# Optimization experiments

Hardware: AMD Instinct MI355X
Metric: run time of the kernel (lower is better)

## Reference

```python
import jax, jax.numpy as jnp
import numpy as np

EPS = 1e-5


def sage_conv(x, src, dst, Wl, Wr, b, n):
    # PyG SAGEConv: out_i = W_l * mean_{j in N(i)} x_j + W_r * x_i + b
    agg = jax.ops.segment_sum(x[src], dst, num_segments=n)  # [N, d]
    deg = jax.ops.segment_sum(jnp.ones_like(src, dtype=x.dtype), dst, num_segments=n)
    agg = agg / jnp.maximum(deg, 1.0)[:, None]
    return agg @ Wl + x @ Wr + b


def setup_inputs() -> dict:
    key = jax.random.key(0)
    ks = jax.random.split(key, 12)
    N, E, D_IN, D_H, D_OUT = 50000, 600000, 128, 128, 64
    x = jax.random.normal(ks[0], (N, D_IN), dtype=jnp.float32)
    edge_index = jax.random.randint(ks[1], (2, E), 0, N, dtype=jnp.int64)
    s_in = 1.0 / np.sqrt(D_IN)
    s_h = 1.0 / np.sqrt(D_H)
    return {
        "x": x,
        "edge_index": edge_index,
        "Wl0": jax.random.normal(ks[2], (D_IN, D_H), jnp.float32) * s_in,
        "Wr0": jax.random.normal(ks[3], (D_IN, D_H), jnp.float32) * s_in,
        "b0": jnp.zeros((D_H,), jnp.float32),
        "Wl1": jax.random.normal(ks[4], (D_H, D_H), jnp.float32) * s_h,
        "Wr1": jax.random.normal(ks[5], (D_H, D_H), jnp.float32) * s_h,
        "b1": jnp.zeros((D_H,), jnp.float32),
        "Wl2": jax.random.normal(ks[6], (D_H, D_OUT), jnp.float32) * s_h,
        "Wr2": jax.random.normal(ks[7], (D_H, D_OUT), jnp.float32) * s_h,
        "b2": jnp.zeros((D_OUT,), jnp.float32),
        "gamma": jnp.ones((D_H,), jnp.float32),
        "beta": jnp.zeros((D_H,), jnp.float32),
    }


def reference(x, edge_index, Wl0, Wr0, b0, Wl1, Wr1, b1, Wl2, Wr2, b2, gamma, beta):
    n = x.shape[0]
    src, dst = edge_index[0], edge_index[1]
    residual = x  # in_channels == hidden_channels -> no residual_transform
    # layer 0: conv + relu (+ dropout as identity in eval)
    h = jax.nn.relu(sage_conv(x, src, dst, Wl0, Wr0, b0, n))
    # middle layer: conv + BN(batch stats) + relu + residual
    h = sage_conv(h, src, dst, Wl1, Wr1, b1, n)
    mu = jnp.mean(h, axis=0)
    var = jnp.var(h, axis=0)  # biased, as in torch BN normalization
    h = (h - mu) * jax.lax.rsqrt(var + EPS) * gamma + beta
    h = jax.nn.relu(h) + residual
    # output layer
    h = sage_conv(h, src, dst, Wl2, Wr2, b2, n)
    return jax.nn.log_softmax(h, axis=-1)
```

## Files before the change

kernel.cpp:

```cpp
#include <hip/hip_runtime.h>
#include <hip/hip_bf16.h>


#define WS_EPS 1e-5f

typedef unsigned short ushort_t;
typedef unsigned int uint_t;
typedef unsigned char uchar_t;
typedef ushort_t ushort8 __attribute__((ext_vector_type(8)));
typedef short short8 __attribute__((ext_vector_type(8)));
typedef float f32x4 __attribute__((ext_vector_type(4)));
typedef _Float16 half2v __attribute__((ext_vector_type(2)));

__device__ __forceinline__ float bf2f(ushort_t u) {
    return __uint_as_float(((uint_t)u) << 16);
}
__device__ __forceinline__ ushort_t f2bf(float f) {
    uint_t u = __float_as_uint(f);
    u = (u + 0x7fffu + ((u >> 16) & 1u)) >> 16;
    return (ushort_t)u;
}
__device__ __forceinline__ uchar_t f2e4m3(float f) {
    _Float16 hf = (_Float16)f;
    uint_t h = (uint_t)__builtin_bit_cast(unsigned short, hf);
    uint_t s = (h >> 8) & 0x80u;
    uint_t r = h & 0x7fffu;
    if (r < 0x2400u) return (uchar_t)0;
    if (r > 0x5F40u) r = 0x5F00u;
    uint_t u = r - 0x2000u;
    uint_t m = (u + 0x3fu + ((u >> 7) & 1u)) >> 7;
    return (uchar_t)(s | m);
}

constexpr int SCHUNK = 4096;

__global__ __launch_bounds__(256) void k_scan_part(const int* __restrict__ deg,
                                                   int* __restrict__ bsum, int n) {
    int t = threadIdx.x;
    int base = blockIdx.x * SCHUNK + t * 16;
    int s = 0;
#pragma unroll
    for (int j = 0; j < 16; ++j) {
        int i = base + j;
        if (i < n) s += deg[i];
    }
#pragma unroll
    for (int d = 1; d < 64; d <<= 1) s += __shfl_xor(s, d);
    __shared__ int wt[4];
    if ((t & 63) == 0) wt[t >> 6] = s;
    __syncthreads();
    if (t == 0) bsum[blockIdx.x] = wt[0] + wt[1] + wt[2] + wt[3];
}

__global__ __launch_bounds__(64) void k_scan_bsum(const int* __restrict__ bsum,
                                                  int* __restrict__ boff,
                                                  int* __restrict__ off_n, int nb) {
    int lane = threadIdx.x;
    int carry = 0;
    for (int base = 0; base < nb; base += 64) {
        int t = base + lane;
        int v = (t < nb) ? bsum[t] : 0;
        int x = v;
#pragma unroll
        for (int d = 1; d < 64; d <<= 1) {
            int y = __shfl_up(x, d);
            if (lane >= d) x += y;
        }
        if (t < nb) boff[t] = carry + x - v;
        carry += __shfl(x, 63);
    }
    if (lane == 0) *off_n = carry;
}

__global__ __launch_bounds__(256) void k_scan_apply(const int* __restrict__ deg,
                                                    const int* __restrict__ boff,
                                                    int* __restrict__ off, int n) {
    int t = threadIdx.x;
    int lane = t & 63, wid = t >> 6;
    int base = blockIdx.x * SCHUNK + t * 16;
    int v[16];
    int s = 0;
#pragma unroll
    for (int j = 0; j < 16; ++j) {
        int i = base + j;
        v[j] = (i < n) ? deg[i] : 0;
        s += v[j];
    }
    int x = s;
#pragma unroll
    for (int d = 1; d < 64; d <<= 1) {
        int y = __shfl_up(x, d);
        if (lane >= d) x += y;
    }
    __shared__ int wtot[4];
    if (lane == 63) wtot[wid] = x;
    __syncthreads();
    int woff = 0;
    for (int wj = 0; wj < wid; ++wj) woff += wtot[wj];
    int run = boff[blockIdx.x] + woff + x - s;
#pragma unroll
    for (int j = 0; j < 16; ++j) {
        int i = base + j;
        if (i < n) off[i] = run;
        run += v[j];
    }
}

__global__ __launch_bounds__(256) void k_scatter(const int* __restrict__ ei,
                                                 const int* __restrict__ off,
                                                 int* __restrict__ cur,
                                                 int* __restrict__ csr, int E) {
    int e = blockIdx.x * 256 + threadIdx.x;
    if (e < E) {
        int d = ei[E + e];
        int s = ei[e];
        int p = atomicAdd(&cur[d], 1);
        csr[off[d] + p] = s;
    }
}

__global__ __launch_bounds__(256) void k_deg_prep(const int* __restrict__ ei,
                                                  int* __restrict__ deg, int E, int eb,
                                                  const float* __restrict__ x,
                                                  ushort_t* __restrict__ xb,
                                                  uchar_t* __restrict__ x8,
                                                  int total2, int nb_cvt,
                                                  const float* __restrict__ Wl0,
                                                  const float* __restrict__ Wr0,
                                                  const float* __restrict__ Wl1,
                                                  const float* __restrict__ Wr1,
                                                  const float* __restrict__ Wl2,
                                                  const float* __restrict__ Wr2,
                                                  ushort_t* __restrict__ wts) {
    int b = blockIdx.x;
    if (b < eb) {
        int e = b * 256 + threadIdx.x;
        if (e < E) atomicAdd(&deg[ei[E + e]], 1);
        return;
    }
    b -= eb;
    if (b < nb_cvt) {
        int i = b * 256 + threadIdx.x;
        if (i >= total2) return;
        float2 v = *(const float2*)&x[(size_t)i * 2];
        uint_t p = (uint_t)f2bf(v.x) | ((uint_t)f2bf(v.y) << 16);
        *(uint_t*)&xb[(size_t)i * 2] = p;
        ushort_t q = (ushort_t)((uint_t)f2e4m3(v.x) | ((uint_t)f2e4m3(v.y) << 8));
        *(ushort_t*)&x8[(size_t)i * 2] = q;
        return;
    }
    int id = (b - nb_cvt) * 256 + threadIdx.x;
    if (id >= 81920) return;
    const float* W;
    int rel, nout, base;
    if (id < 65536) {
        int m = id >> 14;
        rel = id & 16383;
        nout = 128;
        base = m << 14;
        W = (m == 0) ? Wl0 : (m == 1) ? Wr0 : (m == 2) ? Wl1 : Wr1;
    } else {
        int m = (id - 65536) >> 13;
        rel = (id - 65536) & 8191;
        nout = 64;
        base = 65536 + (m << 13);
        W = (m == 0) ? Wl2 : Wr2;
    }
    int c = rel >> 7;
    int k = rel & 127;
    wts[base + rel] = f2bf(W[(size_t)k * nout + c]);
}

template <int EPI>
__global__ __launch_bounds__(256, 3) void k_dgemm(const ushort_t* __restrict__ X1,
                                                  const ushort_t* __restrict__ W1,
                                                  const ushort_t* __restrict__ X2,
                                                  const ushort_t* __restrict__ W2,
                                                  const float* __restrict__ bias,
                                                  ushort_t* __restrict__ outp,
                                                  uchar_t* __restrict__ out8,
                                                  float* __restrict__ stats, int n) {
    constexpr int K = 128, NOUT = 128;
    __shared__ ushort_t Bs[2048 * 8];
    __shared__ float sred[256];

    const int t = threadIdx.x;
    const int lane = t & 63;
    const int r16 = lane & 15, kb = lane >> 4;
    const int half = blockIdx.x & 1;
    const int colbase = half * 64;
    const int w = t >> 6;
    const int sA = (blockIdx.x >> 1) * 8 + w * 2;
    const int sB = sA + 1;

    if (EPI == 1) sred[t] = 0.f;

    ushort8 wreg[8];
#pragma unroll
    for (int u = 0; u < 8; ++u) {
        int slot = u * 256 + t;
        int mat = slot >> 10;
        int rem = slot & 1023;
        int fnks = rem >> 6;
        int l = rem & 63;
        int fn = fnks >> 2, ks = fnks & 3;
        const ushort_t* Wm = mat ? W2 : W1;
        wreg[u] = *(const ushort8*)&Wm[(size_t)(colbase + fn * 16 + (l & 15)) * K +
                                       ks * 32 + (l >> 4) * 8];
    }
    const int rowA = sA * 16 + r16, rowB = sB * 16 + r16;
    const bool okA = rowA < n, okB = rowB < n;
    const size_t xoA = (size_t)rowA * K + kb * 8;
    const size_t xoB = (size_t)rowB * K + kb * 8;
    short8 a1A[4], a2A[4], a1B[4], a2B[4];
#pragma unroll
    for (int ks = 0; ks < 4; ++ks)
        a1A[ks] = okA ? *(const short8*)&X1[xoA + ks * 32] : (short8)0;
#pragma unroll
    for (int ks = 0; ks < 4; ++ks)
        a2A[ks] = okA ? *(const short8*)&X2[xoA + ks * 32] : (short8)0;
#pragma unroll
    for (int ks = 0; ks < 4; ++ks)
        a1B[ks] = okB ? *(const short8*)&X1[xoB + ks * 32] : (short8)0;
#pragma unroll
    for (int ks = 0; ks < 4; ++ks)
        a2B[ks] = okB ? *(const short8*)&X2[xoB + ks * 32] : (short8)0;
#pragma unroll
    for (int u = 0; u < 8; ++u) {
        int slot = u * 256 + t;
        *(ushort8*)&Bs[(size_t)slot * 8] = wreg[u];
    }
    __syncthreads();

    f32x4 accA[4] = {(f32x4)0.f, (f32x4)0.f, (f32x4)0.f, (f32x4)0.f};
    f32x4 accB[4] = {(f32x4)0.f, (f32x4)0.f, (f32x4)0.f, (f32x4)0.f};
#pragma unroll
    for (int ks = 0; ks < 4; ++ks)
#pragma unroll
        for (int fn = 0; fn < 4; ++fn) {
            short8 b = *(const short8*)&Bs[((fn * 4 + ks) * 64 + lane) * 8];
            accA[fn] = __builtin_amdgcn_mfma_f32_16x16x32_bf16(a1A[ks], b, accA[fn], 0, 0, 0);
            accB[fn] = __builtin_amdgcn_mfma_f32_16x16x32_bf16(a1B[ks], b, accB[fn], 0, 0, 0);
        }
#pragma unroll
    for (int ks = 0; ks < 4; ++ks)
#pragma unroll
        for (int fn = 0; fn < 4; ++fn) {
            short8 b = *(const short8*)&Bs[((16 + fn * 4 + ks) * 64 + lane) * 8];
            accA[fn] = __builtin_amdgcn_mfma_f32_16x16x32_bf16(a2A[ks], b, accA[fn], 0, 0, 0);
            accB[fn] = __builtin_amdgcn_mfma_f32_16x16x32_bf16(a2B[ks], b, accB[fn], 0, 0, 0);
        }

    float bcol[4];
#pragma unroll
    for (int fn = 0; fn < 4; ++fn) bcol[fn] = bias[colbase + fn * 16 + r16];

    float ssum[4] = {0.f, 0.f, 0.f, 0.f}, qsum[4] = {0.f, 0.f, 0.f, 0.f};

    {
        const int rb = sA * 16 + kb * 4;
#pragma unroll
        for (int r = 0; r < 4; ++r) {
            int row = rb + r;
            if (row >= n) continue;
#pragma unroll
            for (int fn = 0; fn < 4; ++fn) {
                int col = colbase + fn * 16 + r16;
                float v = accA[fn][r] + bcol[fn];
                if constexpr (EPI == 2) {
                    v = fmaxf(v, 0.f);
                    outp[(size_t)row * NOUT + col] = f2bf(v);
                    out8[(size_t)row * NOUT + col] = f2e4m3(v);
                } else {
                    outp[(size_t)row * NOUT + col] = f2bf(v);
                    ssum[fn] += v;
                    qsum[fn] += v * v;
                }
            }
        }
    }
    {
        const int rb = sB * 16 + kb * 4;
#pragma unroll
        for (int r = 0; r < 4; ++r) {
            int row = rb + r;
            if (row >= n) continue;
#pragma unroll
            for (int fn = 0; fn < 4; ++fn) {
                int col = colbase + fn * 16 + r16;
                float v = accB[fn][r] + bcol[fn];
                if constexpr (EPI == 2) {
                    v = fmaxf(v, 0.f);
                    outp[(size_t)row * NOUT + col] = f2bf(v);
                    out8[(size_t)row * NOUT + col] = f2e4m3(v);
                } else {
                    outp[(size_t)row * NOUT + col] = f2bf(v);
                    ssum[fn] += v;
                    qsum[fn] += v * v;
                }
            }
        }
    }

    if constexpr (EPI == 1) {
#pragma unroll
        for (int fn = 0; fn < 4; ++fn) {
            ssum[fn] += __shfl_xor(ssum[fn], 16);
            ssum[fn] += __shfl_xor(ssum[fn], 32);
            qsum[fn] += __shfl_xor(qsum[fn], 16);
            qsum[fn] += __shfl_xor(qsum[fn], 32);
        }
        if (kb == 0) {
#pragma unroll
            for (int fn = 0; fn < 4; ++fn) {
                int col = colbase + fn * 16 + r16;
                atomicAdd(&sred[col], ssum[fn]);
                atomicAdd(&sred[128 + col], qsum[fn]);
            }
        }
        __syncthreads();
        atomicAdd(&stats[t], sred[t]);
    }
}

__global__ __launch_bounds__(256, 4) void k_cgemm(const ushort_t* __restrict__ H,
                                                  const ushort_t* __restrict__ WL,
                                                  const ushort_t* __restrict__ WR,
                                                  const float* __restrict__ b2,
                                                  ushort_t* __restrict__ A64,
                                                  ushort_t* __restrict__ Tb, int n) {
    constexpr int K = 128;
    __shared__ ushort_t Bs[2048 * 8];

    const int t = threadIdx.x;
    const int lane = t & 63;
    const int r16 = lane & 15, kb = lane >> 4;
    const int strip = blockIdx.x * 4 + (t >> 6);

    ushort8 wreg[8];
#pragma unroll
    for (int u = 0; u < 8; ++u) {
        int slot = u * 256 + t;
        int mat = slot >> 10;
        int rem = slot & 1023;
        int fnks = rem >> 6;
        int l = rem & 63;
        int fn = fnks >> 2, ks = fnks & 3;
        const ushort_t* Wm = mat ? WR : WL;
        wreg[u] = *(const ushort8*)&Wm[(size_t)(fn * 16 + (l & 15)) * K +
                                       ks * 32 + (l >> 4) * 8];
    }
    const int arow = strip * 16 + r16;
    const bool rok = (arow < n);
    const size_t xo = (size_t)arow * K + kb * 8;
    short8 a[4];
#pragma unroll
    for (int ks = 0; ks < 4; ++ks)
        a[ks] = rok ? *(const short8*)&H[xo + ks * 32] : (short8)0;
#pragma unroll
    for (int u = 0; u < 8; ++u) {
        int slot = u * 256 + t;
        *(ushort8*)&Bs[(size_t)slot * 8] = wreg[u];
    }
    __syncthreads();

    f32x4 aL[4] = {(f32x4)0.f, (f32x4)0.f, (f32x4)0.f, (f32x4)0.f};
    f32x4 aR[4] = {(f32x4)0.f, (f32x4)0.f, (f32x4)0.f, (f32x4)0.f};
#pragma unroll
    for (int ks = 0; ks < 4; ++ks)
#pragma unroll
        for (int fn = 0; fn < 4; ++fn) {
            short8 bl = *(const short8*)&Bs[((fn * 4 + ks) * 64 + lane) * 8];
            short8 br = *(const short8*)&Bs[((16 + fn * 4 + ks) * 64 + lane) * 8];
            aL[fn] = __builtin_amdgcn_mfma_f32_16x16x32_bf16(a[ks], bl, aL[fn], 0, 0, 0);
            aR[fn] = __builtin_amdgcn_mfma_f32_16x16x32_bf16(a[ks], br, aR[fn], 0, 0, 0);
        }

    float bcol[4];
#pragma unroll
    for (int fn = 0; fn < 4; ++fn) bcol[fn] = b2[fn * 16 + r16];

    const int rb = strip * 16 + kb * 4;
#pragma unroll
    for (int r = 0; r < 4; ++r) {
        int row = rb + r;
        if (row >= n) continue;
#pragma unroll
        for (int fn = 0; fn < 4; ++fn) {
            int col = fn * 16 + r16;
            A64[(size_t)row * 64 + col] = f2bf(aL[fn][r]);
            Tb[(size_t)row * 64 + col] = f2bf(aR[fn][r] + bcol[fn]);
        }
    }
}

__global__ __launch_bounds__(256) void k_segmean8(const uchar_t* __restrict__ U8,
                                                  const int* __restrict__ off,
                                                  const int* __restrict__ srcs,
                                                  ushort_t* __restrict__ out, int n) {
    int node = blockIdx.x * 32 + (threadIdx.x >> 3);
    int sub = threadIdx.x & 7;
    if (node >= n) return;
    int beg = off[node], end = off[node + 1];
    half2v aE0 = (half2v)0, aE1 = (half2v)0, aE2 = (half2v)0, aE3 = (half2v)0;
    half2v aO0 = (half2v)0, aO1 = (half2v)0, aO2 = (half2v)0, aO3 = (half2v)0;

#define DEC(dw, AE, AO)                                                           \
    {                                                                             \
        uint_t xe = (dw)&0x00ff00ffu;                                             \
        uint_t xo = ((dw) >> 8) & 0x00ff00ffu;                                    \
        uint_t he = ((xe & 0x00800080u) << 8) |                                   \
                    (((xe & 0x007f007fu) << 7) + 0x20002000u);                    \
        uint_t ho = ((xo & 0x00800080u) << 8) |                                   \
                    (((xo & 0x007f007fu) << 7) + 0x20002000u);                    \
        AE += __builtin_bit_cast(half2v, he);                                     \
        AO += __builtin_bit_cast(half2v, ho);                                     \
    }

    auto addrow = [&](int sidx) {
        uint4 v = *(const uint4*)&U8[(size_t)sidx * 128 + sub * 16];
        DEC(v.x, aE0, aO0)
        DEC(v.y, aE1, aO1)
        DEC(v.z, aE2, aO2)
        DEC(v.w, aE3, aO3)
    };
#undef DEC

    int i = beg;
    for (; i + 8 <= end; i += 8) {
        int sv[8];
#pragma unroll
        for (int u = 0; u < 8; ++u) sv[u] = srcs[i + u];
#pragma unroll
        for (int u = 0; u < 8; ++u) addrow(sv[u]);
    }
    for (; i < end; ++i) addrow(srcs[i]);

    int d = end - beg;
    float inv = 1.f / (float)(d > 1 ? d : 1);
    ushort8 o0, o1;
#define PACK(AE, AO, O, IDX)                     \
    O[IDX] = f2bf((float)AE[0] * inv);           \
    O[IDX + 1] = f2bf((float)AO[0] * inv);       \
    O[IDX + 2] = f2bf((float)AE[1] * inv);       \
    O[IDX + 3] = f2bf((float)AO[1] * inv);
    PACK(aE0, aO0, o0, 0)
    PACK(aE1, aO1, o0, 4)
    PACK(aE2, aO2, o1, 0)
    PACK(aE3, aO3, o1, 4)
#undef PACK
    *(ushort8*)&out[(size_t)node * 128 + sub * 16] = o0;
    *(ushort8*)&out[(size_t)node * 128 + sub * 16 + 8] = o1;
}

__global__ __launch_bounds__(256) void k_segmean_lsm(const ushort_t* __restrict__ A64,
                                                     const int* __restrict__ off,
                                                     const int* __restrict__ srcs,
                                                     const ushort_t* __restrict__ Tb,
                                                     float* __restrict__ out, int n) {
    int node = blockIdx.x * 32 + (threadIdx.x >> 3);
    int sub = threadIdx.x & 7;
    if (node >= n) return;
    int beg = off[node], end = off[node + 1];
    float a[8];
#pragma unroll
    for (int j = 0; j < 8; ++j) a[j] = 0.f;
    int i = beg;
    for (; i + 8 <= end; i += 8) {
        int sv[8];
#pragma unroll
        for (int u = 0; u < 8; ++u) sv[u] = srcs[i + u];
#pragma unroll
        for (int u = 0; u < 8; ++u) {
            ushort8 v = *(const ushort8*)&A64[(size_t)sv[u] * 64 + sub * 8];
#pragma unroll
            for (int j = 0; j < 8; ++j) a[j] += bf2f((ushort_t)v[j]);
        }
    }
    for (; i < end; ++i) {
        ushort8 v = *(const ushort8*)&A64[(size_t)srcs[i] * 64 + sub * 8];
#pragma unroll
        for (int j = 0; j < 8; ++j) a[j] += bf2f((ushort_t)v[j]);
    }
    int d = end - beg;
    float inv = 1.f / (float)(d > 1 ? d : 1);
    ushort8 tv = *(const ushort8*)&Tb[(size_t)node * 64 + sub * 8];
    float vv[8];
#pragma unroll
    for (int j = 0; j < 8; ++j) vv[j] = a[j] * inv + bf2f((ushort_t)tv[j]);
    float m = vv[0];
#pragma unroll
    for (int j = 1; j < 8; ++j) m = fmaxf(m, vv[j]);
#pragma unroll
    for (int dd = 1; dd < 8; dd <<= 1) m = fmaxf(m, __shfl_xor(m, dd));
    float e = 0.f;
#pragma unroll
    for (int j = 0; j < 8; ++j) e += expf(vv[j] - m);
#pragma unroll
    for (int dd = 1; dd < 8; dd <<= 1) e += __shfl_xor(e, dd);
    float lg = m + logf(e);
    f32x4 o0, o1;
#pragma unroll
    for (int j = 0; j < 4; ++j) {
        o0[j] = vv[j] - lg;
        o1[j] = vv[4 + j] - lg;
    }
    *(f32x4*)&out[(size_t)node * 64 + sub * 8] = o0;
    *(f32x4*)&out[(size_t)node * 64 + sub * 8 + 4] = o1;
}

__global__ __launch_bounds__(256) void k_bnapply(const ushort_t* __restrict__ P,
                                                 const ushort_t* __restrict__ Xb,
                                                 const float* __restrict__ stats,
                                                 const float* __restrict__ gamma,
                                                 const float* __restrict__ beta,
                                                 ushort_t* __restrict__ H, int n) {
    int i = blockIdx.x * 256 + threadIdx.x;
    if (i >= n * 64) return;
    int nd = i >> 6;
    int c = (i & 63) << 1;
    float inv_n = 1.f / (float)n;
    float mu0 = stats[c] * inv_n, mu1 = stats[c + 1] * inv_n;
    float v0 = stats[128 + c] * inv_n - mu0 * mu0;
    float v1 = stats[128 + c + 1] * inv_n - mu1 * mu1;
    float s0 = rsqrtf(v0 + WS_EPS) * gamma[c];
    float s1 = rsqrtf(v1 + WS_EPS) * gamma[c + 1];
    uint_t pv = *(const uint_t*)&P[(size_t)nd * 128 + c];
    uint_t xv = *(const uint_t*)&Xb[(size_t)nd * 128 + c];
    float p0 = __uint_as_float(pv << 16);
    float p1 = __uint_as_float(pv & 0xffff0000u);
    float x0 = __uint_as_float(xv << 16);
    float x1 = __uint_as_float(xv & 0xffff0000u);
    float h0 = fmaxf((p0 - mu0) * s0 + beta[c], 0.f) + x0;
    float h1 = fmaxf((p1 - mu1) * s1 + beta[c + 1], 0.f) + x1;
    uint_t pk = (uint_t)f2bf(h0) | ((uint_t)f2bf(h1) << 16);
    *(uint_t*)&H[(size_t)nd * 128 + c] = pk;
}

extern "C" void kernel_launch(void* const* d_in, const int* in_sizes, int n_in,
                              void* d_out, int out_size, void* d_ws, size_t ws_size,
                              hipStream_t stream) {
    const float* x     = (const float*)d_in[0];
    const int*   ei    = (const int*)d_in[1];
    const float* Wl0   = (const float*)d_in[2];
    const float* Wr0   = (const float*)d_in[3];
    const float* b0    = (const float*)d_in[4];
    const float* Wl1   = (const float*)d_in[5];
    const float* Wr1   = (const float*)d_in[6];
    const float* b1    = (const float*)d_in[7];
    const float* Wl2   = (const float*)d_in[8];
    const float* Wr2   = (const float*)d_in[9];
    const float* b2    = (const float*)d_in[10];
    const float* gamma = (const float*)d_in[11];
    const float* beta  = (const float*)d_in[12];

    const int n = in_sizes[0] / 128;
    const int E = in_sizes[1] / 2;
    const int nb_scan = (n + SCHUNK - 1) / SCHUNK;

    char* w = (char*)d_ws;
    auto alloc = [&](size_t bytes) -> void* {
        void* p = (void*)w;
        w += (bytes + 255) & ~(size_t)255;
        return p;
    };
    int*      deg   = (int*)alloc((size_t)n * 4);
    int*      cur   = (int*)alloc((size_t)n * 4);
    float*    stats = (float*)alloc(256 * 4);
    size_t    zbytes = (size_t)((char*)w - (char*)deg);
    int*      off   = (int*)alloc(((size_t)n + 1) * 4);
    int*      csr   = (int*)alloc((size_t)E * 4);
    int*      bsum  = (int*)alloc(256 * 4);
    int*      boff  = (int*)alloc(256 * 4);
    ushort_t* wts   = (ushort_t*)alloc((size_t)81920 * 2);
    ushort_t* xb    = (ushort_t*)alloc((size_t)n * 128 * 2);
    uchar_t*  x8    = (uchar_t*)alloc((size_t)n * 128);
    ushort_t* H     = (ushort_t*)alloc((size_t)n * 128 * 2);
    uchar_t*  H8    = (uchar_t*)alloc((size_t)n * 128);
    ushort_t* Pb    = (ushort_t*)alloc((size_t)n * 128 * 2);
    ushort_t* M     = (ushort_t*)alloc((size_t)n * 128 * 2);
    ushort_t* A64   = (ushort_t*)alloc((size_t)n * 64 * 2);
    ushort_t* Tb    = (ushort_t*)alloc((size_t)n * 64 * 2);

    ushort_t* WtL0 = wts;
    ushort_t* WtR0 = wts + 16384;
    ushort_t* WtL1 = wts + 32768;
    ushort_t* WtR1 = wts + 49152;
    ushort_t* WtL2 = wts + 65536;
    ushort_t* WtR2 = wts + 73728;

    hipMemsetAsync(deg, 0, zbytes, stream);

    const int eb = (E + 255) / 256;
    const int nb_cvt = (n * 64 + 255) / 256;
    k_deg_prep<<<eb + nb_cvt + 320, 256, 0, stream>>>(ei, deg, E, eb, x, xb, x8,
                                                      n * 64, nb_cvt,
                                                      Wl0, Wr0, Wl1, Wr1, Wl2, Wr2, wts);
    k_scan_part<<<nb_scan, 256, 0, stream>>>(deg, bsum, n);
    k_scan_bsum<<<1, 64, 0, stream>>>(bsum, boff, off + n, nb_scan);
    k_scan_apply<<<nb_scan, 256, 0, stream>>>(deg, boff, off, n);
    k_scatter<<<(E + 255) / 256, 256, 0, stream>>>(ei, off, cur, csr, E);

    const int strips = (n + 15) / 16;
    const int gb_d = 2 * ((strips + 7) / 8);
    const int gb_c = (strips + 3) / 4;
    const int smb = (n + 31) / 32;

    k_segmean8<<<smb, 256, 0, stream>>>(x8, off, csr, M, n);
    k_dgemm<2><<<gb_d, 256, 0, stream>>>(xb, WtR0, M, WtL0, b0, H, H8, nullptr, n);

    k_segmean8<<<smb, 256, 0, stream>>>(H8, off, csr, M, n);
    k_dgemm<1><<<gb_d, 256, 0, stream>>>(H, WtR1, M, WtL1, b1, Pb, nullptr, stats, n);
    k_bnapply<<<(n * 64 + 255) / 256, 256, 0, stream>>>(Pb, xb, stats, gamma, beta, H, n);

    k_cgemm<<<gb_c, 256, 0, stream>>>(H, WtL2, WtR2, b2, A64, Tb, n);
    k_segmean_lsm<<<smb, 256, 0, stream>>>(A64, off, csr, Tb, (float*)d_out, n);
}
```

Before: 224.9 us.

## Fuse BN-apply into output GEMM and double rows per dgemm wave

```diff
diff --git a/kernel.cpp b/kernel.cpp
--- a/kernel.cpp
+++ b/kernel.cpp
@@ -171,8 +171,42 @@
     wts[base + rel] = f2bf(W[(size_t)k * nout + c]);
 }
 
+#define DG_LOADA(A1, A2, SS)                                                   \
+    {                                                                          \
+        int row_ = (SS)*16 + r16;                                              \
+        bool ok_ = row_ < n;                                                   \
+        size_t xo_ = (size_t)row_ * K + kb * 8;                                \
+        _Pragma("unroll") for (int ks = 0; ks < 4; ++ks)                       \
+            A1[ks] = ok_ ? *(const short8*)&X1[xo_ + ks * 32] : (short8)0;     \
+        _Pragma("unroll") for (int ks = 0; ks < 4; ++ks)                       \
+            A2[ks] = ok_ ? *(const short8*)&X2[xo_ + ks * 32] : (short8)0;     \
+    }
+
+#define DG_EPI(ACC, SS)                                                        \
+    {                                                                          \
+        const int rb_ = (SS)*16 + kb * 4;                                      \
+        _Pragma("unroll") for (int r = 0; r < 4; ++r) {                        \
+            int row_ = rb_ + r;                                                \
+            if (row_ < n) {                                                    \
+                _Pragma("unroll") for (int fn = 0; fn < 4; ++fn) {             \
+                    int col_ = colbase + fn * 16 + r16;                        \
+                    float v_ = ACC[fn][r] + bcol[fn];                          \
+                    if (EPI == 2) {                                            \
+                        v_ = fmaxf(v_, 0.f);                                   \
+                        outp[(size_t)row_ * NOUT + col_] = f2bf(v_);           \
+                        out8[(size_t)row_ * NOUT + col_] = f2e4m3(v_);         \
+                    } else {                                                   \
+                        outp[(size_t)row_ * NOUT + col_] = f2bf(v_);           \
+                        ssum[fn] += v_;                                        \
+                        qsum[fn] += v_ * v_;                                   \
+                    }                                                          \
+                }                                                              \
+            }                                                                  \
+        }                                                                      \
+    }
+
 template <int EPI>
-__global__ __launch_bounds__(256, 3) void k_dgemm(const ushort_t* __restrict__ X1,
+__global__ __launch_bounds__(256, 2) void k_dgemm(const ushort_t* __restrict__ X1,
                                                   const ushort_t* __restrict__ W1,
                                                   const ushort_t* __restrict__ X2,
                                                   const ushort_t* __restrict__ W2,
@@ -190,8 +224,8 @@
     const int half = blockIdx.x & 1;
     const int colbase = half * 64;
     const int w = t >> 6;
-    const int sA = (blockIdx.x >> 1) * 8 + w * 2;
-    const int sB = sA + 1;
+    const int sA = (blockIdx.x >> 1) * 16 + w * 4;
+    const int sB = sA + 1, sC = sA + 2, sD = sA + 3;
 
     if (EPI == 1) sred[t] = 0.f;
 
@@ -208,23 +242,11 @@
         wreg[u] = *(const ushort8*)&Wm[(size_t)(colbase + fn * 16 + (l & 15)) * K +
                                        ks * 32 + (l >> 4) * 8];
     }
-    const int rowA = sA * 16 + r16, rowB = sB * 16 + r16;
-    const bool okA = rowA < n, okB = rowB < n;
-    const size_t xoA = (size_t)rowA * K + kb * 8;
-    const size_t xoB = (size_t)rowB * K + kb * 8;
-    short8 a1A[4], a2A[4], a1B[4], a2B[4];
-#pragma unroll
-    for (int ks = 0; ks < 4; ++ks)
-        a1A[ks] = okA ? *(const short8*)&X1[xoA + ks * 32] : (short8)0;
-#pragma unroll
-    for (int ks = 0; ks < 4; ++ks)
-        a2A[ks] = okA ? *(const short8*)&X2[xoA + ks * 32] : (short8)0;
-#pragma unroll
-    for (int ks = 0; ks < 4; ++ks)
-        a1B[ks] = okB ? *(const short8*)&X1[xoB + ks * 32] : (short8)0;
-#pragma unroll
-    for (int ks = 0; ks < 4; ++ks)
-        a2B[ks] = okB ? *(const short8*)&X2[xoB + ks * 32] : (short8)0;
+    short8 a1A[4], a2A[4], a1B[4], a2B[4], a1C[4], a2C[4], a1D[4], a2D[4];
+    DG_LOADA(a1A, a2A, sA)
+    DG_LOADA(a1B, a2B, sB)
+    DG_LOADA(a1C, a2C, sC)
+    DG_LOADA(a1D, a2D, sD)
 #pragma unroll
     for (int u = 0; u < 8; ++u) {
         int slot = u * 256 + t;
@@ -234,6 +256,8 @@
 
     f32x4 accA[4] = {(f32x4)0.f, (f32x4)0.f, (f32x4)0.f, (f32x4)0.f};
     f32x4 accB[4] = {(f32x4)0.f, (f32x4)0.f, (f32x4)0.f, (f32x4)0.f};
+    f32x4 accC[4] = {(f32x4)0.f, (f32x4)0.f, (f32x4)0.f, (f32x4)0.f};
+    f32x4 accD[4] = {(f32x4)0.f, (f32x4)0.f, (f32x4)0.f, (f32x4)0.f};
 #pragma unroll
     for (int ks = 0; ks < 4; ++ks)
 #pragma unroll
@@ -241,6 +265,8 @@
             short8 b = *(const short8*)&Bs[((fn * 4 + ks) * 64 + lane) * 8];
             accA[fn] = __builtin_amdgcn_mfma_f32_16x16x32_bf16(a1A[ks], b, accA[fn], 0, 0, 0);
             accB[fn] = __builtin_amdgcn_mfma_f32_16x16x32_bf16(a1B[ks], b, accB[fn], 0, 0, 0);
+            accC[fn] = __builtin_amdgcn_mfma_f32_16x16x32_bf16(a1C[ks], b, accC[fn], 0, 0, 0);
+            accD[fn] = __builtin_amdgcn_mfma_f32_16x16x32_bf16(a1D[ks], b, accD[fn], 0, 0, 0);
         }
 #pragma unroll
     for (int ks = 0; ks < 4; ++ks)
@@ -249,6 +275,8 @@
             short8 b = *(const short8*)&Bs[((16 + fn * 4 + ks) * 64 + lane) * 8];
             accA[fn] = __builtin_amdgcn_mfma_f32_16x16x32_bf16(a2A[ks], b, accA[fn], 0, 0, 0);
             accB[fn] = __builtin_amdgcn_mfma_f32_16x16x32_bf16(a2B[ks], b, accB[fn], 0, 0, 0);
+            accC[fn] = __builtin_amdgcn_mfma_f32_16x16x32_bf16(a2C[ks], b, accC[fn], 0, 0, 0);
+            accD[fn] = __builtin_amdgcn_mfma_f32_16x16x32_bf16(a2D[ks], b, accD[fn], 0, 0, 0);
         }
 
     float bcol[4];
@@ -256,51 +284,10 @@
     for (int fn = 0; fn < 4; ++fn) bcol[fn] = bias[colbase + fn * 16 + r16];
 
     float ssum[4] = {0.f, 0.f, 0.f, 0.f}, qsum[4] = {0.f, 0.f, 0.f, 0.f};
-
-    {
-        const int rb = sA * 16 + kb * 4;
-#pragma unroll
-        for (int r = 0; r < 4; ++r) {
-            int row = rb + r;
-            if (row >= n) continue;
-#pragma unroll
-            for (int fn = 0; fn < 4; ++fn) {
-                int col = colbase + fn * 16 + r16;
-                float v = accA[fn][r] + bcol[fn];
-                if constexpr (EPI == 2) {
-                    v = fmaxf(v, 0.f);
-                    outp[(size_t)row * NOUT + col] = f2bf(v);
-                    out8[(size_t)row * NOUT + col] = f2e4m3(v);
-                } else {
-                    outp[(size_t)row * NOUT + col] = f2bf(v);
-                    ssum[fn] += v;
-                    qsum[fn] += v * v;
-                }
-            }
-        }
-    }
-    {
-        const int rb = sB * 16 + kb * 4;
-#pragma unroll
-        for (int r = 0; r < 4; ++r) {
-            int row = rb + r;
-            if (row >= n) continue;
-#pragma unroll
-            for (int fn = 0; fn < 4; ++fn) {
-                int col = colbase + fn * 16 + r16;
-                float v = accB[fn][r] + bcol[fn];
-                if constexpr (EPI == 2) {
-                    v = fmaxf(v, 0.f);
-                    outp[(size_t)row * NOUT + col] = f2bf(v);
-                    out8[(size_t)row * NOUT + col] = f2e4m3(v);
-                } else {
-                    outp[(size_t)row * NOUT + col] = f2bf(v);
-                    ssum[fn] += v;
-                    qsum[fn] += v * v;
-                }
-            }
-        }
-    }
+    DG_EPI(accA, sA)
+    DG_EPI(accB, sB)
+    DG_EPI(accC, sC)
+    DG_EPI(accD, sD)
 
     if constexpr (EPI == 1) {
 #pragma unroll
@@ -323,14 +310,19 @@
     }
 }
 
-__global__ __launch_bounds__(256, 4) void k_cgemm(const ushort_t* __restrict__ H,
-                                                  const ushort_t* __restrict__ WL,
-                                                  const ushort_t* __restrict__ WR,
-                                                  const float* __restrict__ b2,
-                                                  ushort_t* __restrict__ A64,
-                                                  ushort_t* __restrict__ Tb, int n) {
+__global__ __launch_bounds__(256, 4) void k_cgemm_bn(const ushort_t* __restrict__ Pb,
+                                                     const ushort_t* __restrict__ Xb,
+                                                     const float* __restrict__ stats,
+                                                     const float* __restrict__ gamma,
+                                                     const float* __restrict__ beta,
+                                                     const ushort_t* __restrict__ WL,
+                                                     const ushort_t* __restrict__ WR,
+                                                     const float* __restrict__ b2,
+                                                     ushort_t* __restrict__ A64,
+                                                     ushort_t* __restrict__ Tb, int n) {
     constexpr int K = 128;
     __shared__ ushort_t Bs[2048 * 8];
+    __shared__ float st[256];
 
     const int t = threadIdx.x;
     const int lane = t & 63;
@@ -350,19 +342,43 @@
         wreg[u] = *(const ushort8*)&Wm[(size_t)(fn * 16 + (l & 15)) * K +
                                        ks * 32 + (l >> 4) * 8];
     }
+    if (t < 128) {
+        float inv_n = 1.f / (float)n;
+        float mu = stats[t] * inv_n;
+        float var = stats[128 + t] * inv_n - mu * mu;
+        float s = rsqrtf(var + WS_EPS) * gamma[t];
+        st[t] = s;
+        st[128 + t] = beta[t] - mu * s;
+    }
     const int arow = strip * 16 + r16;
     const bool rok = (arow < n);
     const size_t xo = (size_t)arow * K + kb * 8;
-    short8 a[4];
+    short8 pv[4], xv[4];
 #pragma unroll
     for (int ks = 0; ks < 4; ++ks)
-        a[ks] = rok ? *(const short8*)&H[xo + ks * 32] : (short8)0;
+        pv[ks] = rok ? *(const short8*)&Pb[xo + ks * 32] : (short8)0;
+#pragma unroll
+    for (int ks = 0; ks < 4; ++ks)
+        xv[ks] = rok ? *(const short8*)&Xb[xo + ks * 32] : (short8)0;
 #pragma unroll
     for (int u = 0; u < 8; ++u) {
         int slot = u * 256 + t;
         *(ushort8*)&Bs[(size_t)slot * 8] = wreg[u];
     }
     __syncthreads();
+
+    short8 a[4];
+#pragma unroll
+    for (int ks = 0; ks < 4; ++ks) {
+#pragma unroll
+        for (int j = 0; j < 8; ++j) {
+            int c = ks * 32 + kb * 8 + j;
+            float pp = bf2f((ushort_t)pv[ks][j]);
+            float xx = bf2f((ushort_t)xv[ks][j]);
+            float h = fmaxf(pp * st[c] + st[128 + c], 0.f) + xx;
+            a[ks][j] = (short)f2bf(h);
+        }
+    }
 
     f32x4 aL[4] = {(f32x4)0.f, (f32x4)0.f, (f32x4)0.f, (f32x4)0.f};
     f32x4 aR[4] = {(f32x4)0.f, (f32x4)0.f, (f32x4)0.f, (f32x4)0.f};
@@ -507,34 +523,6 @@
     }
     *(f32x4*)&out[(size_t)node * 64 + sub * 8] = o0;
     *(f32x4*)&out[(size_t)node * 64 + sub * 8 + 4] = o1;
-}
-
-__global__ __launch_bounds__(256) void k_bnapply(const ushort_t* __restrict__ P,
-                                                 const ushort_t* __restrict__ Xb,
-                                                 const float* __restrict__ stats,
-                                                 const float* __restrict__ gamma,
-                                                 const float* __restrict__ beta,
-                                                 ushort_t* __restrict__ H, int n) {
-    int i = blockIdx.x * 256 + threadIdx.x;
-    if (i >= n * 64) return;
-    int nd = i >> 6;
-    int c = (i & 63) << 1;
-    float inv_n = 1.f / (float)n;
-    float mu0 = stats[c] * inv_n, mu1 = stats[c + 1] * inv_n;
-    float v0 = stats[128 + c] * inv_n - mu0 * mu0;
-    float v1 = stats[128 + c + 1] * inv_n - mu1 * mu1;
-    float s0 = rsqrtf(v0 + WS_EPS) * gamma[c];
-    float s1 = rsqrtf(v1 + WS_EPS) * gamma[c + 1];
-    uint_t pv = *(const uint_t*)&P[(size_t)nd * 128 + c];
-    uint_t xv = *(const uint_t*)&Xb[(size_t)nd * 128 + c];
-    float p0 = __uint_as_float(pv << 16);
-    float p1 = __uint_as_float(pv & 0xffff0000u);
-    float x0 = __uint_as_float(xv << 16);
-    float x1 = __uint_as_float(xv & 0xffff0000u);
-    float h0 = fmaxf((p0 - mu0) * s0 + beta[c], 0.f) + x0;
-    float h1 = fmaxf((p1 - mu1) * s1 + beta[c + 1], 0.f) + x1;
-    uint_t pk = (uint_t)f2bf(h0) | ((uint_t)f2bf(h1) << 16);
-    *(uint_t*)&H[(size_t)nd * 128 + c] = pk;
 }
 
 extern "C" void kernel_launch(void* const* d_in, const int* in_sizes, int n_in,
@@ -602,7 +590,7 @@
     k_scatter<<<(E + 255) / 256, 256, 0, stream>>>(ei, off, cur, csr, E);
 
     const int strips = (n + 15) / 16;
-    const int gb_d = 2 * ((strips + 7) / 8);
+    const int gb_d = 2 * ((strips + 15) / 16);
     const int gb_c = (strips + 3) / 4;
     const int smb = (n + 31) / 32;
 
@@ -611,8 +599,8 @@
 
     k_segmean8<<<smb, 256, 0, stream>>>(H8, off, csr, M, n);
     k_dgemm<1><<<gb_d, 256, 0, stream>>>(H, WtR1, M, WtL1, b1, Pb, nullptr, stats, n);
-    k_bnapply<<<(n * 64 + 255) / 256, 256, 0, stream>>>(Pb, xb, stats, gamma, beta, H, n);
-
-    k_cgemm<<<gb_c, 256, 0, stream>>>(H, WtL2, WtR2, b2, A64, Tb, n);
+
+    k_cgemm_bn<<<gb_c, 256, 0, stream>>>(Pb, xb, stats, gamma, beta,
+                                         WtL2, WtR2, b2, A64, Tb, n);
     k_segmean_lsm<<<smb, 256, 0, stream>>>(A64, off, csr, Tb, (float*)d_out, n);
 }
```

Result: faster. 205.2 us (-8.8%).
